# Performance work log

Hardware: AMD Instinct MI355X
Metric: run time of the kernel (lower is better)

Reference implementation:

```python
import jax, jax.numpy as jnp
import numpy as np

H = 1024

def setup_inputs() -> dict:
    key = jax.random.key(0)
    ks = jax.random.split(key, 10)
    B, S = 4, 2048
    hidden_states = jax.random.normal(ks[0], (B, S, H), dtype=jnp.float32)
    attention_mask = jnp.zeros((B, S, S), dtype=jnp.float32)
    prosody_mask = jax.random.uniform(ks[1], (B, S, S), dtype=jnp.float32)
    sc = 1.0 / np.sqrt(H)
    Wq = jax.random.normal(ks[2], (H, H), dtype=jnp.float32) * sc
    bq = jnp.zeros((H,), dtype=jnp.float32)
    Wk = jax.random.normal(ks[3], (H, H), dtype=jnp.float32) * sc
    bk = jnp.zeros((H,), dtype=jnp.float32)
    Wv = jax.random.normal(ks[4], (H, H), dtype=jnp.float32) * sc
    bv = jnp.zeros((H,), dtype=jnp.float32)
    prosody_weight = jax.random.normal(ks[5], (1,), dtype=jnp.float32)
    return {"hidden_states": hidden_states, "attention_mask": attention_mask,
            "prosody_mask": prosody_mask, "Wq": Wq, "bq": bq, "Wk": Wk, "bk": bk,
            "Wv": Wv, "bv": bv, "prosody_weight": prosody_weight}

def reference(hidden_states, attention_mask, prosody_mask, Wq, bq, Wk, bk, Wv, bv, prosody_weight):
    # q,k,v: [B,S,H]; torch Linear is x @ W.T + b
    q = jnp.einsum('bsh,oh->bso', hidden_states, Wq) + bq
    k = jnp.einsum('bsh,oh->bso', hidden_states, Wk) + bk
    v = jnp.einsum('bsh,oh->bso', hidden_states, Wv) + bv
    scale = 1.0 / jnp.sqrt(jnp.float32(hidden_states.shape[-1]))
    scores = jnp.einsum('bqh,bkh->bqk', q, k) * scale  # [B,S,S]
    scores = scores + attention_mask + prosody_weight[0] * prosody_mask
    probs = jax.nn.softmax(scores, axis=-1)
    context = jnp.einsum('bqk,bkh->bqh', probs, v)
    return context
```

## Files before the change

kernel.cpp:

```cpp
#include <hip/hip_runtime.h>
#include <hip/hip_bf16.h>
#include <stdint.h>

typedef unsigned short u16;
typedef __attribute__((ext_vector_type(8))) __bf16 bf16x8;
typedef __attribute__((ext_vector_type(4))) float f32x4;
typedef __attribute__((ext_vector_type(8))) u16 u16x8;
typedef __attribute__((ext_vector_type(4))) u16 u16x4;

typedef const __attribute__((address_space(1))) void GV;
typedef __attribute__((address_space(3))) void LV;

__device__ __forceinline__ u16 f2bf(float f) {
  union { float f; uint32_t u; } c; c.f = f;
  uint32_t u = c.u;
  u = u + 0x7FFFu + ((u >> 16) & 1u);
  return (u16)(u >> 16);
}

#define BM 128
#define BN 128
#define BK 32

template<int MODE>
__global__ __launch_bounds__(256) void gemm_bt(
    const u16* __restrict__ A, const u16* __restrict__ B,
    int K, int lda, int ldb,
    long sAb, long sBb,
    float* __restrict__ Cf, int ldc, long sCb,
    u16* __restrict__ Qo, u16* __restrict__ Ko, u16* __restrict__ Vo,
    const float* __restrict__ bias)
{
  const int tid = threadIdx.x;
  const int lane = tid & 63;
  const int w = tid >> 6;
  const int wr = w >> 1, wc = w & 1;
  const int bz = blockIdx.z;
  const u16* Ab = A + (long)bz * sAb;
  const u16* Bb = B + (long)bz * sBb;
  const int row0 = blockIdx.y * BM;
  const int col0 = blockIdx.x * BN;

  __shared__ u16 As[BM][BK];
  __shared__ u16 Bs[BN][BK];

  f32x4 acc[4][4];
#pragma unroll
  for (int i = 0; i < 4; ++i)
#pragma unroll
    for (int j = 0; j < 4; ++j) acc[i][j] = (f32x4)(0.f);

  const int srow = w * 16 + (lane >> 2);
  const int scol = (lane & 3) * 8;
  const int fr = lane & 15;
  const int kq = (lane >> 4) * 8;

  const int nkt = K / BK;
  for (int kt = 0; kt < nkt; ++kt) {
    const int kb = kt * BK;
    __syncthreads();
#pragma unroll
    for (int j = 0; j < 2; ++j) {
      const u16* g = Ab + (long)(row0 + srow + j * 64) * lda + (kb + scol);
      __builtin_amdgcn_global_load_lds((GV*)g, (LV*)(&As[w * 16 + j * 64][0]), 16, 0, 0);
    }
#pragma unroll
    for (int j = 0; j < 2; ++j) {
      const u16* g = Bb + (long)(col0 + srow + j * 64) * ldb + (kb + scol);
      __builtin_amdgcn_global_load_lds((GV*)g, (LV*)(&Bs[w * 16 + j * 64][0]), 16, 0, 0);
    }
    asm volatile("s_waitcnt vmcnt(0)" ::: "memory");
    __syncthreads();

    bf16x8 af[4], bfr[4];
#pragma unroll
    for (int mi = 0; mi < 4; ++mi)
      af[mi] = *(const bf16x8*)(&As[wr * 64 + mi * 16 + fr][kq]);
#pragma unroll
    for (int ni = 0; ni < 4; ++ni)
      bfr[ni] = *(const bf16x8*)(&Bs[wc * 64 + ni * 16 + fr][kq]);
#pragma unroll
    for (int mi = 0; mi < 4; ++mi)
#pragma unroll
      for (int ni = 0; ni < 4; ++ni)
        acc[mi][ni] = __builtin_amdgcn_mfma_f32_16x16x32_bf16(af[mi], bfr[ni], acc[mi][ni], 0, 0, 0);
  }

  const int cr = (lane >> 4) * 4;
  const int cc = lane & 15;
#pragma unroll
  for (int mi = 0; mi < 4; ++mi) {
#pragma unroll
    for (int ni = 0; ni < 4; ++ni) {
      const int gcol = col0 + wc * 64 + ni * 16 + cc;
#pragma unroll
      for (int r = 0; r < 4; ++r) {
        const int grow = row0 + wr * 64 + mi * 16 + cr + r;
        float v = acc[mi][ni][r];
        if (MODE == 0) {
          Cf[(long)bz * sCb + (long)grow * ldc + gcol] = v;
        } else {
          v += bias[gcol];
          u16 h = f2bf(v);
          if (gcol < 1024)      Qo[(long)grow * 1024 + gcol] = h;
          else if (gcol < 2048) Ko[(long)grow * 1024 + (gcol - 1024)] = h;
          else                  Vo[(long)grow * 1024 + (gcol - 2048)] = h;
        }
      }
    }
  }
}

__global__ __launch_bounds__(256) void f32_to_bf16_vec(const float* __restrict__ in,
                                                       u16* __restrict__ o, long n)
{
  long i = ((long)blockIdx.x * 256 + threadIdx.x) * 4;
  if (i < n) {
    float4 v = *(const float4*)(in + i);
    u16x4 r; r[0] = f2bf(v.x); r[1] = f2bf(v.y); r[2] = f2bf(v.z); r[3] = f2bf(v.w);
    *(u16x4*)(o + i) = r;
  }
}

__global__ void concat_bias(const float* __restrict__ bq, const float* __restrict__ bk,
                            const float* __restrict__ bv, float* __restrict__ b)
{
  int i = blockIdx.x * 256 + threadIdx.x;
  if (i < 1024)      b[i] = bq[i];
  else if (i < 2048) b[i] = bk[i - 1024];
  else if (i < 3072) b[i] = bv[i - 2048];
}

__global__ __launch_bounds__(256) void transpose_bf16(const u16* __restrict__ V,
                                                      u16* __restrict__ Vt)
{
  __shared__ u16 t[32][33];
  const int b = blockIdx.z;
  const u16* Vb = V + (long)b * 2097152;
  u16* Vtb = Vt + (long)b * 2097152;
  const int tx = threadIdx.x & 31, ty = threadIdx.x >> 5;
  const int h0 = blockIdx.x * 32, s0 = blockIdx.y * 32;
#pragma unroll
  for (int i = 0; i < 4; ++i)
    t[ty + i * 8][tx] = Vb[(long)(s0 + ty + i * 8) * 1024 + h0 + tx];
  __syncthreads();
#pragma unroll
  for (int i = 0; i < 4; ++i)
    Vtb[(long)(h0 + ty + i * 8) * 2048 + s0 + tx] = t[tx][ty + i * 8];
}

__global__ __launch_bounds__(256) void softmax_rows(
    const float* scores, const float* __restrict__ am,
    const float* __restrict__ pm, const float* __restrict__ pw, u16* P)
{
  const long g = blockIdx.x;
  const int tid = threadIdx.x;
  const int lane = tid & 63;
  const int wv = tid >> 6;
  const float* s = scores + g * 2048;
  const float* a = am + g * 2048;
  const float* p = pm + g * 2048;
  u16* po = (u16*)((char*)P + g * 8192);
  const float wgt = pw[0];

  float sv[8], av[8], pvv[8], v[8];
  *(float4*)&sv[0]  = *(const float4*)(s + tid * 8);
  *(float4*)&sv[4]  = *(const float4*)(s + tid * 8 + 4);
  *(float4*)&av[0]  = *(const float4*)(a + tid * 8);
  *(float4*)&av[4]  = *(const float4*)(a + tid * 8 + 4);
  *(float4*)&pvv[0] = *(const float4*)(p + tid * 8);
  *(float4*)&pvv[4] = *(const float4*)(p + tid * 8 + 4);

  float mx = -3.0e38f;
#pragma unroll
  for (int i = 0; i < 8; ++i) {
    v[i] = fmaf(sv[i], 0.03125f, fmaf(wgt, pvv[i], av[i]));
    mx = fmaxf(mx, v[i]);
  }
#pragma unroll
  for (int off = 32; off >= 1; off >>= 1) mx = fmaxf(mx, __shfl_xor(mx, off, 64));
  __shared__ float rmax[4], rsum[4];
  if (lane == 0) rmax[wv] = mx;
  __syncthreads();
  mx = fmaxf(fmaxf(rmax[0], rmax[1]), fmaxf(rmax[2], rmax[3]));

  float sum = 0.f;
#pragma unroll
  for (int i = 0; i < 8; ++i) { v[i] = __expf(v[i] - mx); sum += v[i]; }
#pragma unroll
  for (int off = 32; off >= 1; off >>= 1) sum += __shfl_xor(sum, off, 64);
  if (lane == 0) rsum[wv] = sum;
  __syncthreads();
  sum = rsum[0] + rsum[1] + rsum[2] + rsum[3];
  const float inv = 1.0f / sum;

  u16x8 o;
#pragma unroll
  for (int i = 0; i < 8; ++i) o[i] = f2bf(v[i] * inv);
  *(u16x8*)(po + tid * 8) = o;
}

extern "C" void kernel_launch(void* const* d_in, const int* in_sizes, int n_in,
                              void* d_out, int out_size, void* d_ws, size_t ws_size,
                              hipStream_t stream) {
  const float* hs = (const float*)d_in[0];
  const float* am = (const float*)d_in[1];
  const float* pm = (const float*)d_in[2];
  const float* Wq = (const float*)d_in[3];
  const float* bq = (const float*)d_in[4];
  const float* Wk = (const float*)d_in[5];
  const float* bk = (const float*)d_in[6];
  const float* Wv = (const float*)d_in[7];
  const float* bv = (const float*)d_in[8];
  const float* pw = (const float*)d_in[9];
  float* out = (float*)d_out;

  char* w = (char*)d_ws;
  u16* X      = (u16*)(w);
  u16* Wqkv   = (u16*)(w + 16777216);
  float* bias = (float*)(w + 23068672);
  u16* Qb     = (u16*)(w + 23085056);
  u16* Kb     = (u16*)(w + 39862272);
  u16* Vb     = (u16*)(w + 56639488);
  float* sc   = (float*)(w + 73416704);
  u16* Vt     = X;
  u16* P      = (u16*)sc;

  hipLaunchKernelGGL(f32_to_bf16_vec, dim3(8192), dim3(256), 0, stream, hs, X, 8388608L);
  hipLaunchKernelGGL(f32_to_bf16_vec, dim3(1024), dim3(256), 0, stream, Wq, Wqkv, 1048576L);
  hipLaunchKernelGGL(f32_to_bf16_vec, dim3(1024), dim3(256), 0, stream, Wk, Wqkv + 1048576, 1048576L);
  hipLaunchKernelGGL(f32_to_bf16_vec, dim3(1024), dim3(256), 0, stream, Wv, Wqkv + 2097152, 1048576L);
  hipLaunchKernelGGL(concat_bias, dim3(12), dim3(256), 0, stream, bq, bk, bv, bias);

  hipLaunchKernelGGL((gemm_bt<1>), dim3(24, 64, 1), dim3(256), 0, stream,
                     X, Wqkv, 1024, 1024, 1024, 0L, 0L,
                     (float*)nullptr, 0, 0L, Qb, Kb, Vb, bias);

  hipLaunchKernelGGL(transpose_bf16, dim3(32, 64, 4), dim3(256), 0, stream, Vb, Vt);

  hipLaunchKernelGGL((gemm_bt<0>), dim3(16, 16, 4), dim3(256), 0, stream,
                     Qb, Kb, 1024, 1024, 1024, 2097152L, 2097152L,
                     sc, 2048, 4194304L,
                     (u16*)nullptr, (u16*)nullptr, (u16*)nullptr, (const float*)nullptr);

  hipLaunchKernelGGL(softmax_rows, dim3(8192), dim3(256), 0, stream, sc, am, pm, pw, P);

  hipLaunchKernelGGL((gemm_bt<0>), dim3(8, 16, 4), dim3(256), 0, stream,
                     P, Vt, 2048, 4096, 2048, 8388608L, 2097152L,
                     out, 1024, 2097152L,
                     (u16*)nullptr, (u16*)nullptr, (u16*)nullptr, (const float*)nullptr);
}
```

Before: 403.1 us.

## Replace GEMM with 256x256 double-buffered swizzled kernel and fuse mask/prep

```diff
diff --git a/kernel.cpp b/kernel.cpp
--- a/kernel.cpp
+++ b/kernel.cpp
@@ -18,87 +18,161 @@
   return (u16)(u >> 16);
 }
 
-#define BM 128
-#define BN 128
-#define BK 32
+#define SBAR do { __builtin_amdgcn_sched_barrier(0); __builtin_amdgcn_s_barrier(); \
+                  __builtin_amdgcn_sched_barrier(0); } while (0)
+#define LGKM0 do { asm volatile("s_waitcnt lgkmcnt(0)" ::: "memory"); \
+                   __builtin_amdgcn_sched_barrier(0); } while (0)
 
 template<int MODE>
-__global__ __launch_bounds__(256) void gemm_bt(
+__global__ __launch_bounds__(512, 2) void gemm256(
     const u16* __restrict__ A, const u16* __restrict__ B,
-    int K, int lda, int ldb,
-    long sAb, long sBb,
+    int K, int lda, int ldb, long sAb, long sBb,
     float* __restrict__ Cf, int ldc, long sCb,
     u16* __restrict__ Qo, u16* __restrict__ Ko, u16* __restrict__ Vo,
-    const float* __restrict__ bias)
+    const float* __restrict__ bias,
+    const float* __restrict__ am, const float* __restrict__ pm,
+    const float* __restrict__ pw)
 {
-  const int tid = threadIdx.x;
+  const int tid  = threadIdx.x;
   const int lane = tid & 63;
-  const int w = tid >> 6;
-  const int wr = w >> 1, wc = w & 1;
-  const int bz = blockIdx.z;
+  const int wid  = tid >> 6;
+  const int wr   = wid >> 2;
+  const int wc   = wid & 3;
+  const int frow = lane & 15;
+  const int kq   = (lane >> 4) * 8;
+  const int bz   = blockIdx.z;
+
+  const int nwg = gridDim.x * gridDim.y;
+  const int wg  = blockIdx.y * gridDim.x + blockIdx.x;
+  const int cpx = nwg >> 3;
+  const int swg = (wg & 7) * cpx + (wg >> 3);
+  const int bx  = swg % gridDim.x;
+  const int by  = swg / gridDim.x;
+
   const u16* Ab = A + (long)bz * sAb;
   const u16* Bb = B + (long)bz * sBb;
-  const int row0 = blockIdx.y * BM;
-  const int col0 = blockIdx.x * BN;
-
-  __shared__ u16 As[BM][BK];
-  __shared__ u16 Bs[BN][BK];
-
-  f32x4 acc[4][4];
-#pragma unroll
-  for (int i = 0; i < 4; ++i)
+  const int row0 = by * 256;
+  const int col0 = bx * 256;
+
+  __shared__ u16 As[2][256][64];
+  __shared__ u16 Bs[2][256][64];
+
+  f32x4 acc[8][4];
+#pragma unroll
+  for (int i = 0; i < 8; ++i)
 #pragma unroll
     for (int j = 0; j < 4; ++j) acc[i][j] = (f32x4)(0.f);
 
-  const int srow = w * 16 + (lane >> 2);
-  const int scol = (lane & 3) * 8;
-  const int fr = lane & 15;
-  const int kq = (lane >> 4) * 8;
-
-  const int nkt = K / BK;
-  for (int kt = 0; kt < nkt; ++kt) {
-    const int kb = kt * BK;
-    __syncthreads();
-#pragma unroll
-    for (int j = 0; j < 2; ++j) {
-      const u16* g = Ab + (long)(row0 + srow + j * 64) * lda + (kb + scol);
-      __builtin_amdgcn_global_load_lds((GV*)g, (LV*)(&As[w * 16 + j * 64][0]), 16, 0, 0);
+  bf16x8 aR[8][2];
+  bf16x8 bR[2][2];
+
+  const int nkt   = K >> 6;
+  const int niter = nkt >> 1;
+
+  const int s_rl  = wid * 8 + (lane >> 3);
+  const int s_ch  = (lane & 7) * 16;
+
+  auto STAGE = [&](const u16* Gb, int ldx, int base0, u16* lb, int half, int kt) {
+#pragma unroll
+    for (int r = 0; r < 2; ++r) {
+      const int rl  = half * 128 + r * 64 + s_rl;
+      const int sc_ = s_ch ^ ((rl & 4) << 3);
+      const u16* g  = Gb + (long)(base0 + rl) * ldx + kt * 64 + (sc_ >> 1);
+      __builtin_amdgcn_global_load_lds((GV*)g,
+          (LV*)((char*)lb + (half * 128 + r * 64 + wid * 8) * 128), 16, 0, 0);
     }
-#pragma unroll
-    for (int j = 0; j < 2; ++j) {
-      const u16* g = Bb + (long)(col0 + srow + j * 64) * ldb + (kb + scol);
-      __builtin_amdgcn_global_load_lds((GV*)g, (LV*)(&Bs[w * 16 + j * 64][0]), 16, 0, 0);
-    }
-    asm volatile("s_waitcnt vmcnt(0)" ::: "memory");
-    __syncthreads();
-
-    bf16x8 af[4], bfr[4];
-#pragma unroll
-    for (int mi = 0; mi < 4; ++mi)
-      af[mi] = *(const bf16x8*)(&As[wr * 64 + mi * 16 + fr][kq]);
-#pragma unroll
-    for (int ni = 0; ni < 4; ++ni)
-      bfr[ni] = *(const bf16x8*)(&Bs[wc * 64 + ni * 16 + fr][kq]);
-#pragma unroll
-    for (int mi = 0; mi < 4; ++mi)
-#pragma unroll
-      for (int ni = 0; ni < 4; ++ni)
-        acc[mi][ni] = __builtin_amdgcn_mfma_f32_16x16x32_bf16(af[mi], bfr[ni], acc[mi][ni], 0, 0, 0);
+  };
+  auto LDA4 = [&](const u16* lb, int mh) {
+#pragma unroll
+    for (int m = 0; m < 4; ++m)
+#pragma unroll
+      for (int ks = 0; ks < 2; ++ks) {
+        const int row = wr * 128 + (mh * 4 + m) * 16 + frow;
+        const int lin = row * 128 + (ks * 32 + kq) * 2;
+        aR[mh * 4 + m][ks] = *(const bf16x8*)((const char*)lb + (lin ^ ((row & 4) << 3)));
+      }
+  };
+  auto LDB2 = [&](const u16* lb, int nh) {
+#pragma unroll
+    for (int n = 0; n < 2; ++n)
+#pragma unroll
+      for (int ks = 0; ks < 2; ++ks) {
+        const int row = wc * 64 + (nh * 2 + n) * 16 + frow;
+        const int lin = row * 128 + (ks * 32 + kq) * 2;
+        bR[n][ks] = *(const bf16x8*)((const char*)lb + (lin ^ ((row & 4) << 3)));
+      }
+  };
+  auto MF = [&](int mh, int nh) {
+    __builtin_amdgcn_s_setprio(1);
+#pragma unroll
+    for (int m = 0; m < 4; ++m)
+#pragma unroll
+      for (int n = 0; n < 2; ++n)
+#pragma unroll
+        for (int ks = 0; ks < 2; ++ks)
+          acc[mh * 4 + m][nh * 2 + n] = __builtin_amdgcn_mfma_f32_16x16x32_bf16(
+              aR[mh * 4 + m][ks], bR[n][ks], acc[mh * 4 + m][nh * 2 + n], 0, 0, 0);
+    __builtin_amdgcn_s_setprio(0);
+  };
+
+  u16* wa0 = &As[0][0][0]; u16* wa1 = &As[1][0][0];
+  u16* wb0 = &Bs[0][0][0]; u16* wb1 = &Bs[1][0][0];
+
+  STAGE(Ab, lda, row0, wa0, 0, 0); STAGE(Ab, lda, row0, wa0, 1, 0);
+  STAGE(Bb, ldb, col0, wb0, 0, 0); STAGE(Bb, ldb, col0, wb0, 1, 0);
+  if (nkt > 1) { STAGE(Ab, lda, row0, wa1, 0, 1); STAGE(Ab, lda, row0, wa1, 1, 1); }
+  asm volatile("s_waitcnt vmcnt(4)" ::: "memory");
+  SBAR;
+
+  for (int i = 0; i < niter; ++i) {
+    const int T = 2 * i;
+    const bool lastI = (i == niter - 1);
+    LDA4(wa0, 0); LDB2(wb0, 0);
+    STAGE(Bb, ldb, col0, wb1, 0, T + 1);
+    SBAR; LGKM0; MF(0, 0); SBAR;
+    LDA4(wa0, 1);
+    STAGE(Bb, ldb, col0, wb1, 1, T + 1);
+    SBAR; LGKM0; MF(1, 0); SBAR;
+    LDB2(wb0, 1);
+    if (T + 2 < nkt) STAGE(Ab, lda, row0, wa0, 0, T + 2);
+    SBAR; LGKM0; MF(0, 1); SBAR;
+    if (T + 2 < nkt) STAGE(Ab, lda, row0, wa0, 1, T + 2);
+    SBAR; MF(1, 1);
+    if (lastI) asm volatile("s_waitcnt vmcnt(0)" ::: "memory");
+    else       asm volatile("s_waitcnt vmcnt(4)" ::: "memory");
+    SBAR;
+    LDA4(wa1, 0); LDB2(wb1, 0);
+    if (T + 2 < nkt) STAGE(Bb, ldb, col0, wb0, 0, T + 2);
+    SBAR; LGKM0; MF(0, 0); SBAR;
+    LDA4(wa1, 1);
+    if (T + 2 < nkt) STAGE(Bb, ldb, col0, wb0, 1, T + 2);
+    SBAR; LGKM0; MF(1, 0); SBAR;
+    LDB2(wb1, 1);
+    if (T + 3 < nkt) STAGE(Ab, lda, row0, wa1, 0, T + 3);
+    SBAR; LGKM0; MF(0, 1); SBAR;
+    if (T + 3 < nkt) STAGE(Ab, lda, row0, wa1, 1, T + 3);
+    SBAR; MF(1, 1);
+    if (!lastI) asm volatile("s_waitcnt vmcnt(4)" ::: "memory");
+    SBAR;
   }
 
   const int cr = (lane >> 4) * 4;
   const int cc = lane & 15;
-#pragma unroll
-  for (int mi = 0; mi < 4; ++mi) {
-#pragma unroll
-    for (int ni = 0; ni < 4; ++ni) {
-      const int gcol = col0 + wc * 64 + ni * 16 + cc;
+  const float wgt = (MODE == 2) ? pw[0] : 0.f;
+#pragma unroll
+  for (int mf = 0; mf < 8; ++mf) {
+#pragma unroll
+    for (int nf = 0; nf < 4; ++nf) {
+      const int gcol = col0 + wc * 64 + nf * 16 + cc;
 #pragma unroll
       for (int r = 0; r < 4; ++r) {
-        const int grow = row0 + wr * 64 + mi * 16 + cr + r;
-        float v = acc[mi][ni][r];
+        const int grow = row0 + wr * 128 + mf * 16 + cr + r;
+        float v = acc[mf][nf][r];
         if (MODE == 0) {
           Cf[(long)bz * sCb + (long)grow * ldc + gcol] = v;
+        } else if (MODE == 2) {
+          const long idx = (long)bz * sCb + (long)grow * ldc + gcol;
+          Cf[idx] = fmaf(v, 0.03125f, fmaf(wgt, pm[idx], am[idx]));
         } else {
           v += bias[gcol];
           u16 h = f2bf(v);
@@ -111,24 +185,24 @@
   }
 }
 
-__global__ __launch_bounds__(256) void f32_to_bf16_vec(const float* __restrict__ in,
-                                                       u16* __restrict__ o, long n)
+__global__ __launch_bounds__(256) void prep_all(
+    const float* __restrict__ hs, const float* __restrict__ Wq,
+    const float* __restrict__ Wk, const float* __restrict__ Wv,
+    const float* __restrict__ bq, const float* __restrict__ bk,
+    const float* __restrict__ bv,
+    u16* __restrict__ X, u16* __restrict__ Wqkv, float* __restrict__ bias)
 {
-  long i = ((long)blockIdx.x * 256 + threadIdx.x) * 4;
-  if (i < n) {
-    float4 v = *(const float4*)(in + i);
-    u16x4 r; r[0] = f2bf(v.x); r[1] = f2bf(v.y); r[2] = f2bf(v.z); r[3] = f2bf(v.w);
-    *(u16x4*)(o + i) = r;
-  }
-}
-
-__global__ void concat_bias(const float* __restrict__ bq, const float* __restrict__ bk,
-                            const float* __restrict__ bv, float* __restrict__ b)
-{
-  int i = blockIdx.x * 256 + threadIdx.x;
-  if (i < 1024)      b[i] = bq[i];
-  else if (i < 2048) b[i] = bk[i - 1024];
-  else if (i < 3072) b[i] = bv[i - 2048];
+  const long t = (long)blockIdx.x * 256 + threadIdx.x;
+  const float* src; u16* dst; long i4;
+  if (t < 2097152L)       { src = hs; dst = X;              i4 = t; }
+  else if (t < 2359296L)  { src = Wq; dst = Wqkv;           i4 = t - 2097152L; }
+  else if (t < 2621440L)  { src = Wk; dst = Wqkv + 1048576; i4 = t - 2359296L; }
+  else                    { src = Wv; dst = Wqkv + 2097152; i4 = t - 2621440L; }
+  const long e = i4 * 4;
+  float4 v = *(const float4*)(src + e);
+  u16x4 rr; rr[0] = f2bf(v.x); rr[1] = f2bf(v.y); rr[2] = f2bf(v.z); rr[3] = f2bf(v.w);
+  *(u16x4*)(dst + e) = rr;
+  if (t < 3072) bias[t] = (t < 1024) ? bq[t] : (t < 2048) ? bk[t - 1024] : bv[t - 2048];
 }
 
 __global__ __launch_bounds__(256) void transpose_bf16(const u16* __restrict__ V,
@@ -150,33 +224,22 @@
 }
 
 __global__ __launch_bounds__(256) void softmax_rows(
-    const float* scores, const float* __restrict__ am,
-    const float* __restrict__ pm, const float* __restrict__ pw, u16* P)
+    const float* __restrict__ scores, u16* __restrict__ P)
 {
   const long g = blockIdx.x;
   const int tid = threadIdx.x;
   const int lane = tid & 63;
   const int wv = tid >> 6;
   const float* s = scores + g * 2048;
-  const float* a = am + g * 2048;
-  const float* p = pm + g * 2048;
-  u16* po = (u16*)((char*)P + g * 8192);
-  const float wgt = pw[0];
-
-  float sv[8], av[8], pvv[8], v[8];
-  *(float4*)&sv[0]  = *(const float4*)(s + tid * 8);
-  *(float4*)&sv[4]  = *(const float4*)(s + tid * 8 + 4);
-  *(float4*)&av[0]  = *(const float4*)(a + tid * 8);
-  *(float4*)&av[4]  = *(const float4*)(a + tid * 8 + 4);
-  *(float4*)&pvv[0] = *(const float4*)(p + tid * 8);
-  *(float4*)&pvv[4] = *(const float4*)(p + tid * 8 + 4);
+  u16* po = P + g * 2048;
+
+  float v[8];
+  *(float4*)&v[0] = *(const float4*)(s + tid * 8);
+  *(float4*)&v[4] = *(const float4*)(s + tid * 8 + 4);
 
   float mx = -3.0e38f;
 #pragma unroll
-  for (int i = 0; i < 8; ++i) {
-    v[i] = fmaf(sv[i], 0.03125f, fmaf(wgt, pvv[i], av[i]));
-    mx = fmaxf(mx, v[i]);
-  }
+  for (int i = 0; i < 8; ++i) mx = fmaxf(mx, v[i]);
 #pragma unroll
   for (int off = 32; off >= 1; off >>= 1) mx = fmaxf(mx, __shfl_xor(mx, off, 64));
   __shared__ float rmax[4], rsum[4];
@@ -224,29 +287,29 @@
   u16* Vb     = (u16*)(w + 56639488);
   float* sc   = (float*)(w + 73416704);
   u16* Vt     = X;
-  u16* P      = (u16*)sc;
-
-  hipLaunchKernelGGL(f32_to_bf16_vec, dim3(8192), dim3(256), 0, stream, hs, X, 8388608L);
-  hipLaunchKernelGGL(f32_to_bf16_vec, dim3(1024), dim3(256), 0, stream, Wq, Wqkv, 1048576L);
-  hipLaunchKernelGGL(f32_to_bf16_vec, dim3(1024), dim3(256), 0, stream, Wk, Wqkv + 1048576, 1048576L);
-  hipLaunchKernelGGL(f32_to_bf16_vec, dim3(1024), dim3(256), 0, stream, Wv, Wqkv + 2097152, 1048576L);
-  hipLaunchKernelGGL(concat_bias, dim3(12), dim3(256), 0, stream, bq, bk, bv, bias);
-
-  hipLaunchKernelGGL((gemm_bt<1>), dim3(24, 64, 1), dim3(256), 0, stream,
+  u16* Pc     = Qb;
+
+  hipLaunchKernelGGL(prep_all, dim3(11264), dim3(256), 0, stream,
+                     hs, Wq, Wk, Wv, bq, bk, bv, X, Wqkv, bias);
+
+  hipLaunchKernelGGL((gemm256<1>), dim3(12, 32, 1), dim3(512), 0, stream,
                      X, Wqkv, 1024, 1024, 1024, 0L, 0L,
-                     (float*)nullptr, 0, 0L, Qb, Kb, Vb, bias);
+                     (float*)nullptr, 0, 0L, Qb, Kb, Vb, bias,
+                     (const float*)nullptr, (const float*)nullptr, (const float*)nullptr);
 
   hipLaunchKernelGGL(transpose_bf16, dim3(32, 64, 4), dim3(256), 0, stream, Vb, Vt);
 
-  hipLaunchKernelGGL((gemm_bt<0>), dim3(16, 16, 4), dim3(256), 0, stream,
+  hipLaunchKernelGGL((gemm256<2>), dim3(8, 8, 4), dim3(512), 0, stream,
                      Qb, Kb, 1024, 1024, 1024, 2097152L, 2097152L,
                      sc, 2048, 4194304L,
-                     (u16*)nullptr, (u16*)nullptr, (u16*)nullptr, (const float*)nullptr);
-
-  hipLaunchKernelGGL(softmax_rows, dim3(8192), dim3(256), 0, stream, sc, am, pm, pw, P);
-
-  hipLaunchKernelGGL((gemm_bt<0>), dim3(8, 16, 4), dim3(256), 0, stream,
-                     P, Vt, 2048, 4096, 2048, 8388608L, 2097152L,
+                     (u16*)nullptr, (u16*)nullptr, (u16*)nullptr, (const float*)nullptr,
+                     am, pm, pw);
+
+  hipLaunchKernelGGL(softmax_rows, dim3(8192), dim3(256), 0, stream, sc, Pc);
+
+  hipLaunchKernelGGL((gemm256<0>), dim3(4, 8, 4), dim3(512), 0, stream,
+                     Pc, Vt, 2048, 2048, 2048, 4194304L, 2097152L,
                      out, 1024, 2097152L,
-                     (u16*)nullptr, (u16*)nullptr, (u16*)nullptr, (const float*)nullptr);
-}
+                     (u16*)nullptr, (u16*)nullptr, (u16*)nullptr, (const float*)nullptr,
+                     (const float*)nullptr, (const float*)nullptr, (const float*)nullptr);
+}
```

New measurement: 437.5 us. 8.6% more time.
